# Kernel tuning notes

Measured on AMD Instinct MI355X. Metric: run time of the kernel, lower is better.

## Reference

```python
import jax, jax.numpy as jnp
import numpy as np

COLOR_SIZE = 8
FILTERS = 64
LAYERS = 4
CUMSUM_NORM = 256 * 256 * 3  # hardcoded in original: /256/256/3


def setup_inputs() -> dict:
    key = jax.random.key(0)
    k0, k1, k2, k3 = jax.random.split(key, 4)
    s = 0.05
    example = jax.random.randint(k0, (4, 256, 256, 3), 0, COLOR_SIZE, dtype=jnp.int32)
    # per-channel Dense stacks: layer 0 has input dim 1, layers 1..3 have input dim FILTERS
    W_in_first = jax.random.normal(k1, (3, 1, FILTERS), dtype=jnp.float32) * s
    b_in_first = jnp.zeros((3, FILTERS), dtype=jnp.float32)
    W_in_rest = jax.random.normal(k2, (LAYERS - 1, 3, FILTERS, FILTERS), dtype=jnp.float32) * s
    b_in_rest = jnp.zeros((LAYERS - 1, 3, FILTERS), dtype=jnp.float32)
    W_final = jax.random.normal(k3, (3, FILTERS, COLOR_SIZE), dtype=jnp.float32) * s
    b_final = jnp.zeros((3, COLOR_SIZE), dtype=jnp.float32)
    return {
        "example": example,
        "W_in_first": W_in_first, "b_in_first": b_in_first,
        "W_in_rest": W_in_rest, "b_in_rest": b_in_rest,
        "W_final": W_final, "b_final": b_final,
    }


def reference(example, W_in_first, b_in_first, W_in_rest, b_in_rest, W_final, b_final):
    # example: [B, H, W, 3] int in [0, COLOR_SIZE)
    x = example.astype(jnp.float32) / COLOR_SIZE * 2.0 - 1.0
    B, H, W, _ = x.shape
    L = H * W
    x = x.reshape(B, L, 3, 1)

    def layer(x, Wl, bl):
        # per-channel dense + relu: [B, L, 3, din] x [3, din, dout] -> [B, L, 3, dout]
        x = jax.nn.relu(jnp.einsum('blcd,cde->blce', x, Wl) + bl)
        # flatten channels into the sequence and take causal running sum
        x = x.reshape(B, L * 3, FILTERS)
        x = jnp.cumsum(x, axis=-2) / CUMSUM_NORM
        return x.reshape(B, L, 3, FILTERS)

    x = layer(x, W_in_first, b_in_first)
    for i in range(LAYERS - 1):
        x = layer(x, W_in_rest[i], b_in_rest[i])

    # final per-channel dense to color logits (no activation)
    x = jnp.einsum('blcd,cde->blce', x, W_final) + b_final
    return x.reshape(B, H, W, 3, COLOR_SIZE)
```

## Files before the change

kernel.cpp:

```cpp
#include <hip/hip_runtime.h>
#include <stdint.h>


#define BB 4
#define SP 65536
#define SS 196608
#define CI 1024
#define NG 16
#define INVN (1.0f / 196608.0f)

typedef __attribute__((ext_vector_type(8))) _Float16 half8;
typedef __attribute__((ext_vector_type(4))) float    f32x4;

__global__ __launch_bounds__(256)
void prep(const int* __restrict__ ex, const float* __restrict__ W0,
          const float* __restrict__ b0, const float* __restrict__ Wr,
          const float* __restrict__ Wfin,
          _Float16* __restrict__ Wt16, _Float16* __restrict__ Wf16p,
          float* __restrict__ Wf32, float* __restrict__ tab32,
          int* __restrict__ Hsub, int* __restrict__ Hqrt,
          float* __restrict__ Gz)
{
    __shared__ int hist[16][24];
    int tid = threadIdx.x, bi = blockIdx.x;
    int b = bi >> 6, g = (bi >> 2) & 15, q = bi & 3;
    for (int i = tid; i < 384; i += 256) hist[i / 24][i % 24] = 0;
    __syncthreads();
    for (int it = 0; it < 4; ++it) {
        int pl = it * 256 + tid;
        const int* ep = ex + ((size_t)b * SP + g * 4096 + q * 1024 + pl) * 3;
        int j = pl >> 6;
        atomicAdd(&hist[j][ep[0]], 1);
        atomicAdd(&hist[j][8 + ep[1]], 1);
        atomicAdd(&hist[j][16 + ep[2]], 1);
    }
    __syncthreads();
    for (int i = tid; i < 384; i += 256) {
        int j = i / 24, cv = i % 24;
        Hsub[(size_t)(b * CI + g * 64 + q * 16 + j) * 24 + cv] = hist[j][cv];
    }
    if (tid < 24) {
        int s = 0;
        for (int j = 0; j < 16; ++j) s += hist[j][tid];
        Hqrt[((size_t)(b * NG + g) * 4 + q) * 24 + tid] = s;
    }
    {
        int i0 = bi * 256 + tid, nth = 256 * 256;
        for (int idx = i0; idx < 12288; idx += nth)
            Gz[idx] = 0.f;
        for (int idx = i0; idx < 36864; idx += nth) {
            int d = idx & 63, f = (idx >> 6) & 63, lc = idx >> 12;
            Wt16[idx] = (_Float16)Wr[(size_t)(lc * 64 + d) * 64 + f];
        }
        for (int idx = i0; idx < 3072; idx += nth) {
            int d = idx & 63, n = (idx >> 6) & 15, c = idx >> 10;
            Wf16p[idx] = (n < 8) ? (_Float16)Wfin[(size_t)(c * 64 + d) * 8 + n]
                                 : (_Float16)0.f;
        }
        for (int idx = i0; idx < 1536; idx += nth) {
            int d = idx & 63, ck = idx >> 6;
            Wf32[idx] = Wfin[(size_t)((ck >> 3) * 64 + d) * 8 + (ck & 7)];
        }
        for (int idx = i0; idx < 1536; idx += nth) {
            int f = idx & 63, v = (idx >> 6) & 7, c = idx >> 9;
            float xv = v * 0.25f - 1.0f;
            tab32[idx] = fmaxf(W0[c * 64 + f] * xv + b0[c * 64 + f], 0.f);
        }
    }
}

__global__ __launch_bounds__(256, 4)
void midA(const int* __restrict__ ex,
          const int* __restrict__ Hsub, const int* __restrict__ Hqrt,
          const float* __restrict__ tab32,
          const _Float16* __restrict__ W16, const float* __restrict__ Wd32,
          const float* __restrict__ bias, _Float16* __restrict__ Y,
          float* __restrict__ A64, float* __restrict__ Ggrp)
{
    __shared__ float stab[1536];
    __shared__ __align__(16) _Float16 bounce3[3][64 * 72];
    __shared__ float segwt[3][4][64];
    __shared__ float basearr[192];
    __shared__ float hpart[4][24];
    __shared__ float carry[64];

    int tid = threadIdx.x, bi = blockIdx.x;
    int b = bi >> 10, ci = bi & 1023, g = ci >> 6, cr = ci & 63;
    int w = tid >> 6, ln = tid & 63, lm = ln & 15, lq = ln >> 4;
    int P0 = ci * 64;

    for (int i = tid; i < 1536; i += 256) stab[i] = tab32[i];
    if (ln < 24) {
        float s = 0.f;
        for (int j = w; j < g; j += 4) {
            const int* hq = Hqrt + ((size_t)(b * NG + j) * 4) * 24 + ln;
            s += (float)(hq[0] + hq[24] + hq[48] + hq[72]);
        }
        const int* hp = Hsub + (size_t)(b * CI + g * 64) * 24 + ln;
        for (int j = w; j < cr; j += 4) s += (float)hp[j * 24];
        hpart[w][ln] = s;
    }
    __syncthreads();

    float y0[3][16];
    {
#pragma unroll
        for (int p = 0; p < 16; ++p) {
            const int* ep = ex + ((size_t)b * SP + P0 + w * 16 + p) * 3;
            y0[0][p] = stab[ep[0] * 64 + ln];
            y0[1][p] = stab[(8 + ep[1]) * 64 + ln];
            y0[2][p] = stab[(16 + ep[2]) * 64 + ln];
        }
#pragma unroll
        for (int c = 0; c < 3; ++c)
#pragma unroll
            for (int p = 1; p < 16; ++p) y0[c][p] += y0[c][p - 1];
#pragma unroll
        for (int c = 0; c < 3; ++c) segwt[c][w][ln] = y0[c][15];
    }
    if (tid < 64) {
        float c0 = 0.f;
#pragma unroll
        for (int cv = 0; cv < 24; ++cv) {
            float cnt = hpart[0][cv] + hpart[1][cv] + hpart[2][cv] + hpart[3][cv];
            c0 += cnt * stab[cv * 64 + tid];
        }
        carry[tid] = c0;
    }
    __syncthreads();

    {
        float off0[3];
#pragma unroll
        for (int c = 0; c < 3; ++c) {
            float o = 0.f;
            for (int w2 = 0; w2 < w; ++w2) o += segwt[c][w2][ln];
            off0[c] = o;
        }
#pragma unroll
        for (int p = 0; p < 16; ++p) {
            float S0 = y0[0][p] + off0[0], S1 = y0[1][p] + off0[1], S2 = y0[2][p] + off0[2];
            float P1 = p ? y0[1][p - 1] + off0[1] : off0[1];
            float P2 = p ? y0[2][p - 1] + off0[2] : off0[2];
            int row = w * 16 + p;
            bounce3[0][row * 72 + ln] = (_Float16)(S0 + P1 + P2);
            bounce3[1][row * 72 + ln] = (_Float16)(S0 + S1 + P2);
            bounce3[2][row * 72 + ln] = (_Float16)(S0 + S1 + S2);
        }
    }
    if (tid < 192) {
        int c = tid >> 6, f = tid & 63;
        const float* wp = Wd32 + (size_t)(c * 64) * 64 + f;
        float a = 0.f;
        for (int d = 0; d < 64; ++d) a += carry[d] * wp[d * 64];
        basearr[tid] = bias[tid] + INVN * a;
    }
    __syncthreads();

    f32x4 acc[3][4];
#pragma unroll
    for (int c = 0; c < 3; ++c) {
        const half8* bb = (const half8*)&bounce3[c][0];
        half8 a0 = bb[(w * 16 + lm) * 9 + lq];
        half8 a1 = bb[(w * 16 + lm) * 9 + 4 + lq];
#pragma unroll
        for (int nt = 0; nt < 4; ++nt) {
            const half8* bp = (const half8*)(W16 + (size_t)(c * 64 + nt * 16 + lm) * 64);
            f32x4 t = {0.f, 0.f, 0.f, 0.f};
            t = __builtin_amdgcn_mfma_f32_16x16x32_f16(a0, bp[lq],     t, 0, 0, 0);
            t = __builtin_amdgcn_mfma_f32_16x16x32_f16(a1, bp[4 + lq], t, 0, 0, 0);
            acc[c][nt] = t;
        }
    }

    float s[3][4][4], wexcl[3][4];
#pragma unroll
    for (int c = 0; c < 3; ++c)
#pragma unroll
        for (int nt = 0; nt < 4; ++nt) {
            float base = basearr[c * 64 + nt * 16 + lm];
            float run = 0.f;
#pragma unroll
            for (int r = 0; r < 4; ++r) {
                float yv = fmaxf(base + INVN * acc[c][nt][r], 0.f);
                run += yv; s[c][nt][r] = run;
            }
            float v = run;
            float t1 = __shfl_up(v, 16); if (lq >= 1) v += t1;
            float t2 = __shfl_up(v, 32); if (lq >= 2) v += t2;
            wexcl[c][nt] = v - run;
            if (lq == 3) segwt[c][w][nt * 16 + lm] = v;
        }
    __syncthreads();

    {
        float off[3][4], tot[3][4];
#pragma unroll
        for (int c = 0; c < 3; ++c)
#pragma unroll
            for (int nt = 0; nt < 4; ++nt) {
                float o = wexcl[c][nt], ts = 0.f;
#pragma unroll
                for (int w2 = 0; w2 < 4; ++w2) {
                    float wv = segwt[c][w2][nt * 16 + lm];
                    ts += wv;
                    if (w2 < w) o += wv;
                }
                off[c][nt] = o; tot[c][nt] = ts;
            }
        if (w == 0 && lq == 0)
#pragma unroll
            for (int nt = 0; nt < 4; ++nt) {
                float t3 = tot[0][nt] + tot[1][nt] + tot[2][nt];
                A64[(size_t)(b * CI + ci) * 64 + nt * 16 + lm] = t3;
                atomicAdd(&Ggrp[(size_t)(b * NG + g) * 64 + nt * 16 + lm], t3);
            }
#pragma unroll
        for (int nt = 0; nt < 4; ++nt)
#pragma unroll
            for (int r = 0; r < 4; ++r) {
                float S0 = off[0][nt] + s[0][nt][r];
                float S1 = off[1][nt] + s[1][nt][r];
                float S2 = off[2][nt] + s[2][nt][r];
                float P1 = off[1][nt] + (r ? s[1][nt][r - 1] : 0.f);
                float P2 = off[2][nt] + (r ? s[2][nt][r - 1] : 0.f);
                int row = w * 16 + lq * 4 + r;
                bounce3[0][row * 72 + nt * 16 + lm] = (_Float16)(S0 + P1 + P2);
                bounce3[1][row * 72 + nt * 16 + lm] = (_Float16)(S0 + S1 + P2);
                bounce3[2][row * 72 + nt * 16 + lm] = (_Float16)(S0 + S1 + S2);
            }
    }
    __syncthreads();
#pragma unroll
    for (int q = 0; q < 6; ++q) {
        int idx = q * 256 + tid;
        int c = idx >> 9, rem = idx & 511;
        int pix = rem >> 3, f8 = rem & 7;
        half8 v = *(const half8*)&bounce3[c][pix * 72 + f8 * 8];
        ((half8*)(Y + ((size_t)(b * 3 + c) * SP + P0 + pix) * 64))[f8] = v;
    }
}

__global__ __launch_bounds__(256, 4)
void midB(const _Float16* Yin, _Float16* Yout,
          const float* __restrict__ A64p, const float* __restrict__ Ggrp_p,
          const _Float16* __restrict__ W16, const float* __restrict__ Wd32,
          const float* __restrict__ bias,
          float* __restrict__ A64, float* __restrict__ Ggrp)
{
    __shared__ __align__(16) _Float16 bounce3[3][64 * 72];
    __shared__ float wtop[3][4][64];
    __shared__ float basearr[192];
    __shared__ float cpart[4][64];
    __shared__ float carry[64];

    int tid = threadIdx.x, bi = blockIdx.x;
    int b = bi >> 10, ci = bi & 1023, g = ci >> 6, cr = ci & 63;
    int w = tid >> 6, ln = tid & 63, lm = ln & 15, lq = ln >> 4;
    int P0 = ci * 64;

    half8 af0[3], af1[3];
#pragma unroll
    for (int c = 0; c < 3; ++c) {
        const half8* ap = (const half8*)(Yin + ((size_t)(b * 3 + c) * SP + P0 + w * 16 + lm) * 64);
        af0[c] = ap[lq]; af1[c] = ap[4 + lq];
    }
    {
        float s = 0.f;
        for (int j = w; j < g; j += 4)
            s += Ggrp_p[(size_t)(b * NG + j) * 64 + ln];
        const float* ap = A64p + (size_t)(b * CI + g * 64) * 64 + ln;
        for (int j = w; j < cr; j += 4) s += ap[j * 64];
        cpart[w][ln] = s;
    }
    __syncthreads();
    if (tid < 64)
        carry[tid] = cpart[0][tid] + cpart[1][tid] + cpart[2][tid] + cpart[3][tid];
    __syncthreads();
    if (tid < 192) {
        int c = tid >> 6, f = tid & 63;
        const float* wp = Wd32 + (size_t)(c * 64) * 64 + f;
        float a = 0.f;
        for (int d = 0; d < 64; ++d) a += carry[d] * wp[d * 64];
        basearr[tid] = bias[tid] + INVN * a;
    }
    __syncthreads();

    f32x4 acc[3][4];
#pragma unroll
    for (int c = 0; c < 3; ++c)
#pragma unroll
        for (int nt = 0; nt < 4; ++nt) {
            const half8* bp = (const half8*)(W16 + (size_t)(c * 64 + nt * 16 + lm) * 64);
            f32x4 t = {0.f, 0.f, 0.f, 0.f};
            t = __builtin_amdgcn_mfma_f32_16x16x32_f16(af0[c], bp[lq],     t, 0, 0, 0);
            t = __builtin_amdgcn_mfma_f32_16x16x32_f16(af1[c], bp[4 + lq], t, 0, 0, 0);
            acc[c][nt] = t;
        }

    float s[3][4][4], wexcl[3][4];
#pragma unroll
    for (int c = 0; c < 3; ++c)
#pragma unroll
        for (int nt = 0; nt < 4; ++nt) {
            float base = basearr[c * 64 + nt * 16 + lm];
            float run = 0.f;
#pragma unroll
            for (int r = 0; r < 4; ++r) {
                float yv = fmaxf(base + INVN * acc[c][nt][r], 0.f);
                run += yv; s[c][nt][r] = run;
            }
            float v = run;
            float t1 = __shfl_up(v, 16); if (lq >= 1) v += t1;
            float t2 = __shfl_up(v, 32); if (lq >= 2) v += t2;
            wexcl[c][nt] = v - run;
            if (lq == 3) wtop[c][w][nt * 16 + lm] = v;
        }
    __syncthreads();

    {
        float off[3][4], tot[3][4];
#pragma unroll
        for (int c = 0; c < 3; ++c)
#pragma unroll
            for (int nt = 0; nt < 4; ++nt) {
                float o = wexcl[c][nt], ts = 0.f;
#pragma unroll
                for (int w2 = 0; w2 < 4; ++w2) {
                    float wv = wtop[c][w2][nt * 16 + lm];
                    ts += wv;
                    if (w2 < w) o += wv;
                }
                off[c][nt] = o; tot[c][nt] = ts;
            }
        if (w == 0 && lq == 0)
#pragma unroll
            for (int nt = 0; nt < 4; ++nt) {
                float t3 = tot[0][nt] + tot[1][nt] + tot[2][nt];
                A64[(size_t)(b * CI + ci) * 64 + nt * 16 + lm] = t3;
                atomicAdd(&Ggrp[(size_t)(b * NG + g) * 64 + nt * 16 + lm], t3);
            }
#pragma unroll
        for (int nt = 0; nt < 4; ++nt)
#pragma unroll
            for (int r = 0; r < 4; ++r) {
                float S0 = off[0][nt] + s[0][nt][r];
                float S1 = off[1][nt] + s[1][nt][r];
                float S2 = off[2][nt] + s[2][nt][r];
                float P1 = off[1][nt] + (r ? s[1][nt][r - 1] : 0.f);
                float P2 = off[2][nt] + (r ? s[2][nt][r - 1] : 0.f);
                int row = w * 16 + lq * 4 + r;
                bounce3[0][row * 72 + nt * 16 + lm] = (_Float16)(S0 + P1 + P2);
                bounce3[1][row * 72 + nt * 16 + lm] = (_Float16)(S0 + S1 + P2);
                bounce3[2][row * 72 + nt * 16 + lm] = (_Float16)(S0 + S1 + S2);
            }
    }
    __syncthreads();
#pragma unroll
    for (int q = 0; q < 6; ++q) {
        int idx = q * 256 + tid;
        int c = idx >> 9, rem = idx & 511;
        int pix = rem >> 3, f8 = rem & 7;
        half8 v = *(const half8*)&bounce3[c][pix * 72 + f8 * 8];
        ((half8*)(Yout + ((size_t)(b * 3 + c) * SP + P0 + pix) * 64))[f8] = v;
    }
}

__global__ __launch_bounds__(256, 4)
void midC(const _Float16* __restrict__ Yin,
          const float* __restrict__ A64p, const float* __restrict__ Ggrp_p,
          const _Float16* __restrict__ W16, const float* __restrict__ Wd32,
          const float* __restrict__ bias,
          const _Float16* __restrict__ Wf16p, const float* __restrict__ bfin,
          float* __restrict__ out, float* __restrict__ A64, float* __restrict__ Ggrp)
{
    __shared__ __align__(16) _Float16 bounce3[3][64 * 72];
    __shared__ float wtop[3][4][64];
    __shared__ float basearr[192];
    __shared__ float cpart[4][64];
    __shared__ float carry[64];
    __shared__ __align__(16) float outst[64 * 28];

    int tid = threadIdx.x, bi = blockIdx.x;
    int b = bi >> 10, ci = bi & 1023, g = ci >> 6, cr = ci & 63;
    int w = tid >> 6, ln = tid & 63, lm = ln & 15, lq = ln >> 4;
    int P0 = ci * 64;

    half8 af0[3], af1[3];
#pragma unroll
    for (int c = 0; c < 3; ++c) {
        const half8* ap = (const half8*)(Yin + ((size_t)(b * 3 + c) * SP + P0 + w * 16 + lm) * 64);
        af0[c] = ap[lq]; af1[c] = ap[4 + lq];
    }
    {
        float s = 0.f;
        for (int j = w; j < g; j += 4)
            s += Ggrp_p[(size_t)(b * NG + j) * 64 + ln];
        const float* ap = A64p + (size_t)(b * CI + g * 64) * 64 + ln;
        for (int j = w; j < cr; j += 4) s += ap[j * 64];
        cpart[w][ln] = s;
    }
    __syncthreads();
    if (tid < 64)
        carry[tid] = cpart[0][tid] + cpart[1][tid] + cpart[2][tid] + cpart[3][tid];
    __syncthreads();
    if (tid < 192) {
        int c = tid >> 6, f = tid & 63;
        const float* wp = Wd32 + (size_t)(c * 64) * 64 + f;
        float a = 0.f;
        for (int d = 0; d < 64; ++d) a += carry[d] * wp[d * 64];
        basearr[tid] = bias[tid] + INVN * a;
    }
    __syncthreads();

    f32x4 acc[3][4];
#pragma unroll
    for (int c = 0; c < 3; ++c)
#pragma unroll
        for (int nt = 0; nt < 4; ++nt) {
            const half8* bp = (const half8*)(W16 + (size_t)(c * 64 + nt * 16 + lm) * 64);
            f32x4 t = {0.f, 0.f, 0.f, 0.f};
            t = __builtin_amdgcn_mfma_f32_16x16x32_f16(af0[c], bp[lq],     t, 0, 0, 0);
            t = __builtin_amdgcn_mfma_f32_16x16x32_f16(af1[c], bp[4 + lq], t, 0, 0, 0);
            acc[c][nt] = t;
        }

    float s[3][4][4], wexcl[3][4];
#pragma unroll
    for (int c = 0; c < 3; ++c)
#pragma unroll
        for (int nt = 0; nt < 4; ++nt) {
            float base = basearr[c * 64 + nt * 16 + lm];
            float run = 0.f;
#pragma unroll
            for (int r = 0; r < 4; ++r) {
                float yv = fmaxf(base + INVN * acc[c][nt][r], 0.f);
                run += yv; s[c][nt][r] = run;
            }
            float v = run;
            float t1 = __shfl_up(v, 16); if (lq >= 1) v += t1;
            float t2 = __shfl_up(v, 32); if (lq >= 2) v += t2;
            wexcl[c][nt] = v - run;
            if (lq == 3) wtop[c][w][nt * 16 + lm] = v;
        }
    __syncthreads();

    {
        float off[3][4], tot[3][4];
#pragma unroll
        for (int c = 0; c < 3; ++c)
#pragma unroll
            for (int nt = 0; nt < 4; ++nt) {
                float o = wexcl[c][nt], ts = 0.f;
#pragma unroll
                for (int w2 = 0; w2 < 4; ++w2) {
                    float wv = wtop[c][w2][nt * 16 + lm];
                    ts += wv;
                    if (w2 < w) o += wv;
                }
                off[c][nt] = o; tot[c][nt] = ts;
            }
        if (w == 0 && lq == 0)
#pragma unroll
            for (int nt = 0; nt < 4; ++nt) {
                float t3 = tot[0][nt] + tot[1][nt] + tot[2][nt];
                A64[(size_t)(b * CI + ci) * 64 + nt * 16 + lm] = t3;
                atomicAdd(&Ggrp[(size_t)(b * NG + g) * 64 + nt * 16 + lm], t3);
            }
#pragma unroll
        for (int nt = 0; nt < 4; ++nt)
#pragma unroll
            for (int r = 0; r < 4; ++r) {
                float S0 = off[0][nt] + s[0][nt][r];
                float S1 = off[1][nt] + s[1][nt][r];
                float S2 = off[2][nt] + s[2][nt][r];
                float P1 = off[1][nt] + (r ? s[1][nt][r - 1] : 0.f);
                float P2 = off[2][nt] + (r ? s[2][nt][r - 1] : 0.f);
                int row = w * 16 + lq * 4 + r;
                bounce3[0][row * 72 + nt * 16 + lm] = (_Float16)(S0 + P1 + P2);
                bounce3[1][row * 72 + nt * 16 + lm] = (_Float16)(S0 + S1 + P2);
                bounce3[2][row * 72 + nt * 16 + lm] = (_Float16)(S0 + S1 + S2);
            }
    }
    __syncthreads();

#pragma unroll
    for (int c = 0; c < 3; ++c) {
        const half8* bb = (const half8*)&bounce3[c][0];
        half8 fa0 = bb[(w * 16 + lm) * 9 + lq];
        half8 fa1 = bb[(w * 16 + lm) * 9 + 4 + lq];
        const half8* fb = (const half8*)(Wf16p + (size_t)(c * 16 + lm) * 64);
        f32x4 t = {0.f, 0.f, 0.f, 0.f};
        t = __builtin_amdgcn_mfma_f32_16x16x32_f16(fa0, fb[lq],     t, 0, 0, 0);
        t = __builtin_amdgcn_mfma_f32_16x16x32_f16(fa1, fb[4 + lq], t, 0, 0, 0);
        if (lm < 8) {
            float bz = bfin[c * 8 + lm];
#pragma unroll
            for (int r = 0; r < 4; ++r)
                outst[(w * 16 + lq * 4 + r) * 28 + c * 8 + lm] = bz + INVN * t[r];
        }
    }
    __syncthreads();
    {
        float4* obase = (float4*)(out + ((size_t)b * SS + (size_t)P0 * 3) * 8);
#pragma unroll
        for (int k = 0; k < 2; ++k) {
            int idx = k * 256 + tid;
            if (idx < 384) {
                int pix = idx / 6, sub = (idx % 6) * 4;
                obase[idx] = *(const float4*)&outst[pix * 28 + sub];
            }
        }
    }
}

__global__ __launch_bounds__(256, 4)
void fixk(const float* __restrict__ A64p, const float* __restrict__ Ggrp_p,
          const float* __restrict__ Wf32, float* __restrict__ out)
{
    __shared__ float cpart[4][64];
    __shared__ float carry[64];
    __shared__ float part[24][8];
    __shared__ float vfix[24];
    int tid = threadIdx.x, bi = blockIdx.x;
    int b = bi >> 10, ci = bi & 1023, g = ci >> 6, cr = ci & 63;
    int w = tid >> 6, ln = tid & 63;
    int P0 = ci * 64;

    {
        float s = 0.f;
        for (int j = w; j < g; j += 4)
            s += Ggrp_p[(size_t)(b * NG + j) * 64 + ln];
        const float* ap = A64p + (size_t)(b * CI + g * 64) * 64 + ln;
        for (int j = w; j < cr; j += 4) s += ap[j * 64];
        cpart[w][ln] = s;
    }
    __syncthreads();
    if (tid < 64)
        carry[tid] = cpart[0][tid] + cpart[1][tid] + cpart[2][tid] + cpart[3][tid];
    __syncthreads();
    if (tid < 192) {
        int ck = tid >> 3, sg = tid & 7;
        const float* wp = Wf32 + ck * 64 + sg * 8;
        const float* cp = carry + sg * 8;
        float vf = 0.f;
#pragma unroll
        for (int d = 0; d < 8; ++d) vf += cp[d] * wp[d];
        part[ck][sg] = vf;
    }
    __syncthreads();
    if (tid < 24) {
        float vf = 0.f;
#pragma unroll
        for (int j = 0; j < 8; ++j) vf += part[tid][j];
        vfix[tid] = INVN * vf;
    }
    __syncthreads();
    float4* obase = (float4*)(out + ((size_t)b * SS + (size_t)P0 * 3) * 8);
#pragma unroll
    for (int k = 0; k < 2; ++k) {
        int idx = k * 256 + tid;
        if (idx < 384) {
            int sub = (idx % 6) * 4;
            float4 v = obase[idx];
            v.x += vfix[sub];
            v.y += vfix[sub + 1];
            v.z += vfix[sub + 2];
            v.w += vfix[sub + 3];
            obase[idx] = v;
        }
    }
}

extern "C" void kernel_launch(void* const* d_in, const int* in_sizes, int n_in,
                              void* d_out, int out_size, void* d_ws, size_t ws_size,
                              hipStream_t stream)
{
    const int*   ex   = (const int*)d_in[0];
    const float* W0   = (const float*)d_in[1];
    const float* b0   = (const float*)d_in[2];
    const float* Wr   = (const float*)d_in[3];
    const float* br   = (const float*)d_in[4];
    const float* Wfin = (const float*)d_in[5];
    const float* bfin = (const float*)d_in[6];
    float* out = (float*)d_out;

    char* ws = (char*)d_ws;
    size_t off = 0;
    _Float16* Y = (_Float16*)(ws + off); off += (size_t)BB * 3 * SP * 64 * 2;
    float* Ggrp1 = (float*)(ws + off); off += (size_t)BB * NG * 64 * 4;
    float* Ggrp2 = (float*)(ws + off); off += (size_t)BB * NG * 64 * 4;
    float* Ggrp3 = (float*)(ws + off); off += (size_t)BB * NG * 64 * 4;
    float* A64_1 = (float*)(ws + off); off += (size_t)BB * CI * 64 * 4;
    float* A64_2 = (float*)(ws + off); off += (size_t)BB * CI * 64 * 4;
    float* A64_3 = (float*)(ws + off); off += (size_t)BB * CI * 64 * 4;
    int* Hsub = (int*)(ws + off); off += (size_t)BB * CI * 24 * 4;
    int* Hqrt = (int*)(ws + off); off += (size_t)BB * NG * 4 * 24 * 4;
    _Float16* Wt16  = (_Float16*)(ws + off); off += 36864 * 2;
    _Float16* Wf16p = (_Float16*)(ws + off); off += 3072 * 2;
    float* Wf32  = (float*)(ws + off); off += 1536 * 4;
    float* tab32 = (float*)(ws + off); off += 1536 * 4;

    prep<<<256, 256, 0, stream>>>(ex, W0, b0, Wr, Wfin,
                                  Wt16, Wf16p, Wf32, tab32,
                                  Hsub, Hqrt, Ggrp1);
    midA<<<4096, 256, 0, stream>>>(ex, Hsub, Hqrt, tab32,
                                   Wt16, Wr, br, Y, A64_1, Ggrp1);
    midB<<<4096, 256, 0, stream>>>(Y, Y, A64_1, Ggrp1,
                                   Wt16 + 12288, Wr + 12288, br + 192,
                                   A64_2, Ggrp2);
    midC<<<4096, 256, 0, stream>>>(Y, A64_2, Ggrp2,
                                   Wt16 + 24576, Wr + 24576, br + 384,
                                   Wf16p, bfin, out, A64_3, Ggrp3);
    fixk<<<4096, 256, 0, stream>>>(A64_3, Ggrp3, Wf32, out);
}
```

Baseline: 358.6 us.

## Process two 64-pixel chunks per block to amortize carry and base setup

```diff
diff --git a/kernel.cpp b/kernel.cpp
--- a/kernel.cpp
+++ b/kernel.cpp
@@ -80,14 +80,15 @@
     __shared__ float stab[1536];
     __shared__ __align__(16) _Float16 bounce3[3][64 * 72];
     __shared__ float segwt[3][4][64];
-    __shared__ float basearr[192];
+    __shared__ float basearr[2][192];
     __shared__ float hpart[4][24];
-    __shared__ float carry[64];
+    __shared__ float hrow[24];
+    __shared__ float carry[2][64];
 
     int tid = threadIdx.x, bi = blockIdx.x;
-    int b = bi >> 10, ci = bi & 1023, g = ci >> 6, cr = ci & 63;
+    int b = bi >> 9, cp2 = bi & 511;
+    int ci0 = cp2 * 2, g = ci0 >> 6, cr0 = ci0 & 63;
     int w = tid >> 6, ln = tid & 63, lm = ln & 15, lq = ln >> 4;
-    int P0 = ci * 64;
 
     for (int i = tid; i < 1536; i += 256) stab[i] = tab32[i];
     if (ln < 24) {
@@ -97,13 +98,44 @@
             s += (float)(hq[0] + hq[24] + hq[48] + hq[72]);
         }
         const int* hp = Hsub + (size_t)(b * CI + g * 64) * 24 + ln;
-        for (int j = w; j < cr; j += 4) s += (float)hp[j * 24];
+        for (int j = w; j < cr0; j += 4) s += (float)hp[j * 24];
         hpart[w][ln] = s;
     }
-    __syncthreads();
-
-    float y0[3][16];
-    {
+    if (tid < 24) hrow[tid] = (float)Hsub[(size_t)(b * CI + ci0) * 24 + tid];
+    __syncthreads();
+
+    if (tid < 64) {
+        float c0 = 0.f, c1 = 0.f;
+#pragma unroll
+        for (int cv = 0; cv < 24; ++cv) {
+            float cnt = hpart[0][cv] + hpart[1][cv] + hpart[2][cv] + hpart[3][cv];
+            float sv = stab[cv * 64 + tid];
+            c0 += cnt * sv;
+            c1 += (cnt + hrow[cv]) * sv;
+        }
+        carry[0][tid] = c0; carry[1][tid] = c1;
+    }
+    __syncthreads();
+
+    if (tid < 192) {
+        int c = tid >> 6, f = tid & 63;
+        const float* wp = Wd32 + (size_t)(c * 64) * 64 + f;
+        float a0 = 0.f, a1 = 0.f;
+        for (int d = 0; d < 64; ++d) {
+            float wv = wp[d * 64];
+            a0 += carry[0][d] * wv; a1 += carry[1][d] * wv;
+        }
+        float bz = bias[tid];
+        basearr[0][tid] = bz + INVN * a0;
+        basearr[1][tid] = bz + INVN * a1;
+    }
+    __syncthreads();
+
+#pragma unroll 1
+    for (int pq = 0; pq < 2; ++pq) {
+        int ci = ci0 + pq, P0 = ci * 64;
+
+        float y0[3][16];
 #pragma unroll
         for (int p = 0; p < 16; ++p) {
             const int* ep = ex + ((size_t)b * SP + P0 + w * 16 + p) * 3;
@@ -117,127 +149,111 @@
             for (int p = 1; p < 16; ++p) y0[c][p] += y0[c][p - 1];
 #pragma unroll
         for (int c = 0; c < 3; ++c) segwt[c][w][ln] = y0[c][15];
-    }
-    if (tid < 64) {
-        float c0 = 0.f;
-#pragma unroll
-        for (int cv = 0; cv < 24; ++cv) {
-            float cnt = hpart[0][cv] + hpart[1][cv] + hpart[2][cv] + hpart[3][cv];
-            c0 += cnt * stab[cv * 64 + tid];
-        }
-        carry[tid] = c0;
-    }
-    __syncthreads();
-
-    {
-        float off0[3];
+        __syncthreads();
+
+        {
+            float off0[3];
+#pragma unroll
+            for (int c = 0; c < 3; ++c) {
+                float o = 0.f;
+                for (int w2 = 0; w2 < w; ++w2) o += segwt[c][w2][ln];
+                off0[c] = o;
+            }
+#pragma unroll
+            for (int p = 0; p < 16; ++p) {
+                float S0 = y0[0][p] + off0[0], S1 = y0[1][p] + off0[1], S2 = y0[2][p] + off0[2];
+                float P1 = p ? y0[1][p - 1] + off0[1] : off0[1];
+                float P2 = p ? y0[2][p - 1] + off0[2] : off0[2];
+                int row = w * 16 + p;
+                bounce3[0][row * 72 + ln] = (_Float16)(S0 + P1 + P2);
+                bounce3[1][row * 72 + ln] = (_Float16)(S0 + S1 + P2);
+                bounce3[2][row * 72 + ln] = (_Float16)(S0 + S1 + S2);
+            }
+        }
+        __syncthreads();
+
+        f32x4 acc[3][4];
 #pragma unroll
         for (int c = 0; c < 3; ++c) {
-            float o = 0.f;
-            for (int w2 = 0; w2 < w; ++w2) o += segwt[c][w2][ln];
-            off0[c] = o;
-        }
-#pragma unroll
-        for (int p = 0; p < 16; ++p) {
-            float S0 = y0[0][p] + off0[0], S1 = y0[1][p] + off0[1], S2 = y0[2][p] + off0[2];
-            float P1 = p ? y0[1][p - 1] + off0[1] : off0[1];
-            float P2 = p ? y0[2][p - 1] + off0[2] : off0[2];
-            int row = w * 16 + p;
-            bounce3[0][row * 72 + ln] = (_Float16)(S0 + P1 + P2);
-            bounce3[1][row * 72 + ln] = (_Float16)(S0 + S1 + P2);
-            bounce3[2][row * 72 + ln] = (_Float16)(S0 + S1 + S2);
-        }
-    }
-    if (tid < 192) {
-        int c = tid >> 6, f = tid & 63;
-        const float* wp = Wd32 + (size_t)(c * 64) * 64 + f;
-        float a = 0.f;
-        for (int d = 0; d < 64; ++d) a += carry[d] * wp[d * 64];
-        basearr[tid] = bias[tid] + INVN * a;
-    }
-    __syncthreads();
-
-    f32x4 acc[3][4];
-#pragma unroll
-    for (int c = 0; c < 3; ++c) {
-        const half8* bb = (const half8*)&bounce3[c][0];
-        half8 a0 = bb[(w * 16 + lm) * 9 + lq];
-        half8 a1 = bb[(w * 16 + lm) * 9 + 4 + lq];
-#pragma unroll
-        for (int nt = 0; nt < 4; ++nt) {
-            const half8* bp = (const half8*)(W16 + (size_t)(c * 64 + nt * 16 + lm) * 64);
-            f32x4 t = {0.f, 0.f, 0.f, 0.f};
-            t = __builtin_amdgcn_mfma_f32_16x16x32_f16(a0, bp[lq],     t, 0, 0, 0);
-            t = __builtin_amdgcn_mfma_f32_16x16x32_f16(a1, bp[4 + lq], t, 0, 0, 0);
-            acc[c][nt] = t;
-        }
-    }
-
-    float s[3][4][4], wexcl[3][4];
-#pragma unroll
-    for (int c = 0; c < 3; ++c)
-#pragma unroll
-        for (int nt = 0; nt < 4; ++nt) {
-            float base = basearr[c * 64 + nt * 16 + lm];
-            float run = 0.f;
-#pragma unroll
-            for (int r = 0; r < 4; ++r) {
-                float yv = fmaxf(base + INVN * acc[c][nt][r], 0.f);
-                run += yv; s[c][nt][r] = run;
-            }
-            float v = run;
-            float t1 = __shfl_up(v, 16); if (lq >= 1) v += t1;
-            float t2 = __shfl_up(v, 32); if (lq >= 2) v += t2;
-            wexcl[c][nt] = v - run;
-            if (lq == 3) segwt[c][w][nt * 16 + lm] = v;
-        }
-    __syncthreads();
-
-    {
-        float off[3][4], tot[3][4];
+            const half8* bb = (const half8*)&bounce3[c][0];
+            half8 a0 = bb[(w * 16 + lm) * 9 + lq];
+            half8 a1 = bb[(w * 16 + lm) * 9 + 4 + lq];
+#pragma unroll
+            for (int nt = 0; nt < 4; ++nt) {
+                const half8* bp = (const half8*)(W16 + (size_t)(c * 64 + nt * 16 + lm) * 64);
+                f32x4 t = {0.f, 0.f, 0.f, 0.f};
+                t = __builtin_amdgcn_mfma_f32_16x16x32_f16(a0, bp[lq],     t, 0, 0, 0);
+                t = __builtin_amdgcn_mfma_f32_16x16x32_f16(a1, bp[4 + lq], t, 0, 0, 0);
+                acc[c][nt] = t;
+            }
+        }
+
+        float s[3][4][4], wexcl[3][4];
 #pragma unroll
         for (int c = 0; c < 3; ++c)
 #pragma unroll
             for (int nt = 0; nt < 4; ++nt) {
-                float o = wexcl[c][nt], ts = 0.f;
-#pragma unroll
-                for (int w2 = 0; w2 < 4; ++w2) {
-                    float wv = segwt[c][w2][nt * 16 + lm];
-                    ts += wv;
-                    if (w2 < w) o += wv;
-                }
-                off[c][nt] = o; tot[c][nt] = ts;
-            }
-        if (w == 0 && lq == 0)
-#pragma unroll
-            for (int nt = 0; nt < 4; ++nt) {
-                float t3 = tot[0][nt] + tot[1][nt] + tot[2][nt];
-                A64[(size_t)(b * CI + ci) * 64 + nt * 16 + lm] = t3;
-                atomicAdd(&Ggrp[(size_t)(b * NG + g) * 64 + nt * 16 + lm], t3);
-            }
-#pragma unroll
-        for (int nt = 0; nt < 4; ++nt)
-#pragma unroll
-            for (int r = 0; r < 4; ++r) {
-                float S0 = off[0][nt] + s[0][nt][r];
-                float S1 = off[1][nt] + s[1][nt][r];
-                float S2 = off[2][nt] + s[2][nt][r];
-                float P1 = off[1][nt] + (r ? s[1][nt][r - 1] : 0.f);
-                float P2 = off[2][nt] + (r ? s[2][nt][r - 1] : 0.f);
-                int row = w * 16 + lq * 4 + r;
-                bounce3[0][row * 72 + nt * 16 + lm] = (_Float16)(S0 + P1 + P2);
-                bounce3[1][row * 72 + nt * 16 + lm] = (_Float16)(S0 + S1 + P2);
-                bounce3[2][row * 72 + nt * 16 + lm] = (_Float16)(S0 + S1 + S2);
-            }
-    }
-    __syncthreads();
-#pragma unroll
-    for (int q = 0; q < 6; ++q) {
-        int idx = q * 256 + tid;
-        int c = idx >> 9, rem = idx & 511;
-        int pix = rem >> 3, f8 = rem & 7;
-        half8 v = *(const half8*)&bounce3[c][pix * 72 + f8 * 8];
-        ((half8*)(Y + ((size_t)(b * 3 + c) * SP + P0 + pix) * 64))[f8] = v;
+                float base = basearr[pq][c * 64 + nt * 16 + lm];
+                float run = 0.f;
+#pragma unroll
+                for (int r = 0; r < 4; ++r) {
+                    float yv = fmaxf(base + INVN * acc[c][nt][r], 0.f);
+                    run += yv; s[c][nt][r] = run;
+                }
+                float v = run;
+                float t1 = __shfl_up(v, 16); if (lq >= 1) v += t1;
+                float t2 = __shfl_up(v, 32); if (lq >= 2) v += t2;
+                wexcl[c][nt] = v - run;
+                if (lq == 3) segwt[c][w][nt * 16 + lm] = v;
+            }
+        __syncthreads();
+
+        {
+            float off[3][4], tot[3][4];
+#pragma unroll
+            for (int c = 0; c < 3; ++c)
+#pragma unroll
+                for (int nt = 0; nt < 4; ++nt) {
+                    float o = wexcl[c][nt], ts = 0.f;
+#pragma unroll
+                    for (int w2 = 0; w2 < 4; ++w2) {
+                        float wv = segwt[c][w2][nt * 16 + lm];
+                        ts += wv;
+                        if (w2 < w) o += wv;
+                    }
+                    off[c][nt] = o; tot[c][nt] = ts;
+                }
+            if (w == 0 && lq == 0)
+#pragma unroll
+                for (int nt = 0; nt < 4; ++nt) {
+                    float t3 = tot[0][nt] + tot[1][nt] + tot[2][nt];
+                    A64[(size_t)(b * CI + ci) * 64 + nt * 16 + lm] = t3;
+                    atomicAdd(&Ggrp[(size_t)(b * NG + g) * 64 + nt * 16 + lm], t3);
+                }
+#pragma unroll
+            for (int nt = 0; nt < 4; ++nt)
+#pragma unroll
+                for (int r = 0; r < 4; ++r) {
+                    float S0 = off[0][nt] + s[0][nt][r];
+                    float S1 = off[1][nt] + s[1][nt][r];
+                    float S2 = off[2][nt] + s[2][nt][r];
+                    float P1 = off[1][nt] + (r ? s[1][nt][r - 1] : 0.f);
+                    float P2 = off[2][nt] + (r ? s[2][nt][r - 1] : 0.f);
+                    int row = w * 16 + lq * 4 + r;
+                    bounce3[0][row * 72 + nt * 16 + lm] = (_Float16)(S0 + P1 + P2);
+                    bounce3[1][row * 72 + nt * 16 + lm] = (_Float16)(S0 + S1 + P2);
+                    bounce3[2][row * 72 + nt * 16 + lm] = (_Float16)(S0 + S1 + S2);
+                }
+        }
+        __syncthreads();
+#pragma unroll
+        for (int q = 0; q < 6; ++q) {
+            int idx = q * 256 + tid;
+            int c = idx >> 9, rem = idx & 511;
+            int pix = rem >> 3, f8 = rem & 7;
+            half8 v = *(const half8*)&bounce3[c][pix * 72 + f8 * 8];
+            ((half8*)(Y + ((size_t)(b * 3 + c) * SP + P0 + pix) * 64))[f8] = v;
+        }
     }
 }
 
@@ -250,119 +266,134 @@
 {
     __shared__ __align__(16) _Float16 bounce3[3][64 * 72];
     __shared__ float wtop[3][4][64];
-    __shared__ float basearr[192];
+    __shared__ float basearr[2][192];
     __shared__ float cpart[4][64];
-    __shared__ float carry[64];
+    __shared__ float carry[2][64];
 
     int tid = threadIdx.x, bi = blockIdx.x;
-    int b = bi >> 10, ci = bi & 1023, g = ci >> 6, cr = ci & 63;
+    int b = bi >> 9, cp2 = bi & 511;
+    int ci0 = cp2 * 2, g = ci0 >> 6, cr0 = ci0 & 63;
     int w = tid >> 6, ln = tid & 63, lm = ln & 15, lq = ln >> 4;
-    int P0 = ci * 64;
-
-    half8 af0[3], af1[3];
-#pragma unroll
-    for (int c = 0; c < 3; ++c) {
-        const half8* ap = (const half8*)(Yin + ((size_t)(b * 3 + c) * SP + P0 + w * 16 + lm) * 64);
-        af0[c] = ap[lq]; af1[c] = ap[4 + lq];
-    }
+
     {
         float s = 0.f;
         for (int j = w; j < g; j += 4)
             s += Ggrp_p[(size_t)(b * NG + j) * 64 + ln];
         const float* ap = A64p + (size_t)(b * CI + g * 64) * 64 + ln;
-        for (int j = w; j < cr; j += 4) s += ap[j * 64];
+        for (int j = w; j < cr0; j += 4) s += ap[j * 64];
         cpart[w][ln] = s;
     }
     __syncthreads();
-    if (tid < 64)
-        carry[tid] = cpart[0][tid] + cpart[1][tid] + cpart[2][tid] + cpart[3][tid];
+    if (tid < 64) {
+        float c0 = cpart[0][tid] + cpart[1][tid] + cpart[2][tid] + cpart[3][tid];
+        carry[0][tid] = c0;
+        carry[1][tid] = c0 + A64p[(size_t)(b * CI + ci0) * 64 + tid];
+    }
     __syncthreads();
     if (tid < 192) {
         int c = tid >> 6, f = tid & 63;
         const float* wp = Wd32 + (size_t)(c * 64) * 64 + f;
-        float a = 0.f;
-        for (int d = 0; d < 64; ++d) a += carry[d] * wp[d * 64];
-        basearr[tid] = bias[tid] + INVN * a;
-    }
-    __syncthreads();
-
-    f32x4 acc[3][4];
-#pragma unroll
-    for (int c = 0; c < 3; ++c)
-#pragma unroll
-        for (int nt = 0; nt < 4; ++nt) {
-            const half8* bp = (const half8*)(W16 + (size_t)(c * 64 + nt * 16 + lm) * 64);
-            f32x4 t = {0.f, 0.f, 0.f, 0.f};
-            t = __builtin_amdgcn_mfma_f32_16x16x32_f16(af0[c], bp[lq],     t, 0, 0, 0);
-            t = __builtin_amdgcn_mfma_f32_16x16x32_f16(af1[c], bp[4 + lq], t, 0, 0, 0);
-            acc[c][nt] = t;
-        }
-
-    float s[3][4][4], wexcl[3][4];
-#pragma unroll
-    for (int c = 0; c < 3; ++c)
-#pragma unroll
-        for (int nt = 0; nt < 4; ++nt) {
-            float base = basearr[c * 64 + nt * 16 + lm];
-            float run = 0.f;
-#pragma unroll
-            for (int r = 0; r < 4; ++r) {
-                float yv = fmaxf(base + INVN * acc[c][nt][r], 0.f);
-                run += yv; s[c][nt][r] = run;
-            }
-            float v = run;
-            float t1 = __shfl_up(v, 16); if (lq >= 1) v += t1;
-            float t2 = __shfl_up(v, 32); if (lq >= 2) v += t2;
-            wexcl[c][nt] = v - run;
-            if (lq == 3) wtop[c][w][nt * 16 + lm] = v;
-        }
-    __syncthreads();
-
-    {
-        float off[3][4], tot[3][4];
+        float a0 = 0.f, a1 = 0.f;
+        for (int d = 0; d < 64; ++d) {
+            float wv = wp[d * 64];
+            a0 += carry[0][d] * wv; a1 += carry[1][d] * wv;
+        }
+        float bz = bias[tid];
+        basearr[0][tid] = bz + INVN * a0;
+        basearr[1][tid] = bz + INVN * a1;
+    }
+    __syncthreads();
+
+#pragma unroll 1
+    for (int pq = 0; pq < 2; ++pq) {
+        int ci = ci0 + pq, P0 = ci * 64;
+
+        half8 af0[3], af1[3];
+#pragma unroll
+        for (int c = 0; c < 3; ++c) {
+            const half8* ap = (const half8*)(Yin + ((size_t)(b * 3 + c) * SP + P0 + w * 16 + lm) * 64);
+            af0[c] = ap[lq]; af1[c] = ap[4 + lq];
+        }
+
+        f32x4 acc[3][4];
 #pragma unroll
         for (int c = 0; c < 3; ++c)
 #pragma unroll
             for (int nt = 0; nt < 4; ++nt) {
-                float o = wexcl[c][nt], ts = 0.f;
-#pragma unroll
-                for (int w2 = 0; w2 < 4; ++w2) {
-                    float wv = wtop[c][w2][nt * 16 + lm];
-                    ts += wv;
-                    if (w2 < w) o += wv;
-                }
-                off[c][nt] = o; tot[c][nt] = ts;
-            }
-        if (w == 0 && lq == 0)
+                const half8* bp = (const half8*)(W16 + (size_t)(c * 64 + nt * 16 + lm) * 64);
+                f32x4 t = {0.f, 0.f, 0.f, 0.f};
+                t = __builtin_amdgcn_mfma_f32_16x16x32_f16(af0[c], bp[lq],     t, 0, 0, 0);
+                t = __builtin_amdgcn_mfma_f32_16x16x32_f16(af1[c], bp[4 + lq], t, 0, 0, 0);
+                acc[c][nt] = t;
+            }
+
+        float s[3][4][4], wexcl[3][4];
+#pragma unroll
+        for (int c = 0; c < 3; ++c)
 #pragma unroll
             for (int nt = 0; nt < 4; ++nt) {
-                float t3 = tot[0][nt] + tot[1][nt] + tot[2][nt];
-                A64[(size_t)(b * CI + ci) * 64 + nt * 16 + lm] = t3;
-                atomicAdd(&Ggrp[(size_t)(b * NG + g) * 64 + nt * 16 + lm], t3);
-            }
-#pragma unroll
-        for (int nt = 0; nt < 4; ++nt)
-#pragma unroll
-            for (int r = 0; r < 4; ++r) {
-                float S0 = off[0][nt] + s[0][nt][r];
-                float S1 = off[1][nt] + s[1][nt][r];
-                float S2 = off[2][nt] + s[2][nt][r];
-                float P1 = off[1][nt] + (r ? s[1][nt][r - 1] : 0.f);
-                float P2 = off[2][nt] + (r ? s[2][nt][r - 1] : 0.f);
-                int row = w * 16 + lq * 4 + r;
-                bounce3[0][row * 72 + nt * 16 + lm] = (_Float16)(S0 + P1 + P2);
-                bounce3[1][row * 72 + nt * 16 + lm] = (_Float16)(S0 + S1 + P2);
-                bounce3[2][row * 72 + nt * 16 + lm] = (_Float16)(S0 + S1 + S2);
-            }
-    }
-    __syncthreads();
-#pragma unroll
-    for (int q = 0; q < 6; ++q) {
-        int idx = q * 256 + tid;
-        int c = idx >> 9, rem = idx & 511;
-        int pix = rem >> 3, f8 = rem & 7;
-        half8 v = *(const half8*)&bounce3[c][pix * 72 + f8 * 8];
-        ((half8*)(Yout + ((size_t)(b * 3 + c) * SP + P0 + pix) * 64))[f8] = v;
+                float base = basearr[pq][c * 64 + nt * 16 + lm];
+                float run = 0.f;
+#pragma unroll
+                for (int r = 0; r < 4; ++r) {
+                    float yv = fmaxf(base + INVN * acc[c][nt][r], 0.f);
+                    run += yv; s[c][nt][r] = run;
+                }
+                float v = run;
+                float t1 = __shfl_up(v, 16); if (lq >= 1) v += t1;
+                float t2 = __shfl_up(v, 32); if (lq >= 2) v += t2;
+                wexcl[c][nt] = v - run;
+                if (lq == 3) wtop[c][w][nt * 16 + lm] = v;
+            }
+        __syncthreads();
+
+        {
+            float off[3][4], tot[3][4];
+#pragma unroll
+            for (int c = 0; c < 3; ++c)
+#pragma unroll
+                for (int nt = 0; nt < 4; ++nt) {
+                    float o = wexcl[c][nt], ts = 0.f;
+#pragma unroll
+                    for (int w2 = 0; w2 < 4; ++w2) {
+                        float wv = wtop[c][w2][nt * 16 + lm];
+                        ts += wv;
+                        if (w2 < w) o += wv;
+                    }
+                    off[c][nt] = o; tot[c][nt] = ts;
+                }
+            if (w == 0 && lq == 0)
+#pragma unroll
+                for (int nt = 0; nt < 4; ++nt) {
+                    float t3 = tot[0][nt] + tot[1][nt] + tot[2][nt];
+                    A64[(size_t)(b * CI + ci) * 64 + nt * 16 + lm] = t3;
+                    atomicAdd(&Ggrp[(size_t)(b * NG + g) * 64 + nt * 16 + lm], t3);
+                }
+#pragma unroll
+            for (int nt = 0; nt < 4; ++nt)
+#pragma unroll
+                for (int r = 0; r < 4; ++r) {
+                    float S0 = off[0][nt] + s[0][nt][r];
+                    float S1 = off[1][nt] + s[1][nt][r];
+                    float S2 = off[2][nt] + s[2][nt][r];
+                    float P1 = off[1][nt] + (r ? s[1][nt][r - 1] : 0.f);
+                    float P2 = off[2][nt] + (r ? s[2][nt][r - 1] : 0.f);
+                    int row = w * 16 + lq * 4 + r;
+                    bounce3[0][row * 72 + nt * 16 + lm] = (_Float16)(S0 + P1 + P2);
+                    bounce3[1][row * 72 + nt * 16 + lm] = (_Float16)(S0 + S1 + P2);
+                    bounce3[2][row * 72 + nt * 16 + lm] = (_Float16)(S0 + S1 + S2);
+                }
+        }
+        __syncthreads();
+#pragma unroll
+        for (int q = 0; q < 6; ++q) {
+            int idx = q * 256 + tid;
+            int c = idx >> 9, rem = idx & 511;
+            int pix = rem >> 3, f8 = rem & 7;
+            half8 v = *(const half8*)&bounce3[c][pix * 72 + f8 * 8];
+            ((half8*)(Yout + ((size_t)(b * 3 + c) * SP + P0 + pix) * 64))[f8] = v;
+        }
+        if (pq == 0) __syncthreads();
     }
 }
 
@@ -376,141 +407,156 @@
 {
     __shared__ __align__(16) _Float16 bounce3[3][64 * 72];
     __shared__ float wtop[3][4][64];
-    __shared__ float basearr[192];
-    __shared__ float cpart[4][64];
-    __shared__ float carry[64];
+    __shared__ float basearr[2][192];
     __shared__ __align__(16) float outst[64 * 28];
+    float (*cpart)[64] = (float (*)[64])outst;
+    float (*carry)[64] = (float (*)[64])(outst + 256);
 
     int tid = threadIdx.x, bi = blockIdx.x;
-    int b = bi >> 10, ci = bi & 1023, g = ci >> 6, cr = ci & 63;
+    int b = bi >> 9, cp2 = bi & 511;
+    int ci0 = cp2 * 2, g = ci0 >> 6, cr0 = ci0 & 63;
     int w = tid >> 6, ln = tid & 63, lm = ln & 15, lq = ln >> 4;
-    int P0 = ci * 64;
-
-    half8 af0[3], af1[3];
-#pragma unroll
-    for (int c = 0; c < 3; ++c) {
-        const half8* ap = (const half8*)(Yin + ((size_t)(b * 3 + c) * SP + P0 + w * 16 + lm) * 64);
-        af0[c] = ap[lq]; af1[c] = ap[4 + lq];
-    }
+
     {
         float s = 0.f;
         for (int j = w; j < g; j += 4)
             s += Ggrp_p[(size_t)(b * NG + j) * 64 + ln];
         const float* ap = A64p + (size_t)(b * CI + g * 64) * 64 + ln;
-        for (int j = w; j < cr; j += 4) s += ap[j * 64];
+        for (int j = w; j < cr0; j += 4) s += ap[j * 64];
         cpart[w][ln] = s;
     }
     __syncthreads();
-    if (tid < 64)
-        carry[tid] = cpart[0][tid] + cpart[1][tid] + cpart[2][tid] + cpart[3][tid];
+    if (tid < 64) {
+        float c0 = cpart[0][tid] + cpart[1][tid] + cpart[2][tid] + cpart[3][tid];
+        carry[0][tid] = c0;
+        carry[1][tid] = c0 + A64p[(size_t)(b * CI + ci0) * 64 + tid];
+    }
     __syncthreads();
     if (tid < 192) {
         int c = tid >> 6, f = tid & 63;
         const float* wp = Wd32 + (size_t)(c * 64) * 64 + f;
-        float a = 0.f;
-        for (int d = 0; d < 64; ++d) a += carry[d] * wp[d * 64];
-        basearr[tid] = bias[tid] + INVN * a;
-    }
-    __syncthreads();
-
-    f32x4 acc[3][4];
-#pragma unroll
-    for (int c = 0; c < 3; ++c)
-#pragma unroll
-        for (int nt = 0; nt < 4; ++nt) {
-            const half8* bp = (const half8*)(W16 + (size_t)(c * 64 + nt * 16 + lm) * 64);
+        float a0 = 0.f, a1 = 0.f;
+        for (int d = 0; d < 64; ++d) {
+            float wv = wp[d * 64];
+            a0 += carry[0][d] * wv; a1 += carry[1][d] * wv;
+        }
+        float bz = bias[tid];
+        basearr[0][tid] = bz + INVN * a0;
+        basearr[1][tid] = bz + INVN * a1;
+    }
+    __syncthreads();
+
+#pragma unroll 1
+    for (int pq = 0; pq < 2; ++pq) {
+        int ci = ci0 + pq, P0 = ci * 64;
+
+        half8 af0[3], af1[3];
+#pragma unroll
+        for (int c = 0; c < 3; ++c) {
+            const half8* ap = (const half8*)(Yin + ((size_t)(b * 3 + c) * SP + P0 + w * 16 + lm) * 64);
+            af0[c] = ap[lq]; af1[c] = ap[4 + lq];
+        }
+
+        f32x4 acc[3][4];
+#pragma unroll
+        for (int c = 0; c < 3; ++c)
+#pragma unroll
+            for (int nt = 0; nt < 4; ++nt) {
+                const half8* bp = (const half8*)(W16 + (size_t)(c * 64 + nt * 16 + lm) * 64);
+                f32x4 t = {0.f, 0.f, 0.f, 0.f};
+                t = __builtin_amdgcn_mfma_f32_16x16x32_f16(af0[c], bp[lq],     t, 0, 0, 0);
+                t = __builtin_amdgcn_mfma_f32_16x16x32_f16(af1[c], bp[4 + lq], t, 0, 0, 0);
+                acc[c][nt] = t;
+            }
+
+        float s[3][4][4], wexcl[3][4];
+#pragma unroll
+        for (int c = 0; c < 3; ++c)
+#pragma unroll
+            for (int nt = 0; nt < 4; ++nt) {
+                float base = basearr[pq][c * 64 + nt * 16 + lm];
+                float run = 0.f;
+#pragma unroll
+                for (int r = 0; r < 4; ++r) {
+                    float yv = fmaxf(base + INVN * acc[c][nt][r], 0.f);
+                    run += yv; s[c][nt][r] = run;
+                }
+                float v = run;
+                float t1 = __shfl_up(v, 16); if (lq >= 1) v += t1;
+                float t2 = __shfl_up(v, 32); if (lq >= 2) v += t2;
+                wexcl[c][nt] = v - run;
+                if (lq == 3) wtop[c][w][nt * 16 + lm] = v;
+            }
+        __syncthreads();
+
+        {
+            float off[3][4], tot[3][4];
+#pragma unroll
+            for (int c = 0; c < 3; ++c)
+#pragma unroll
+                for (int nt = 0; nt < 4; ++nt) {
+                    float o = wexcl[c][nt], ts = 0.f;
+#pragma unroll
+                    for (int w2 = 0; w2 < 4; ++w2) {
+                        float wv = wtop[c][w2][nt * 16 + lm];
+                        ts += wv;
+                        if (w2 < w) o += wv;
+                    }
+                    off[c][nt] = o; tot[c][nt] = ts;
+                }
+            if (w == 0 && lq == 0)
+#pragma unroll
+                for (int nt = 0; nt < 4; ++nt) {
+                    float t3 = tot[0][nt] + tot[1][nt] + tot[2][nt];
+                    A64[(size_t)(b * CI + ci) * 64 + nt * 16 + lm] = t3;
+                    atomicAdd(&Ggrp[(size_t)(b * NG + g) * 64 + nt * 16 + lm], t3);
+                }
+#pragma unroll
+            for (int nt = 0; nt < 4; ++nt)
+#pragma unroll
+                for (int r = 0; r < 4; ++r) {
+                    float S0 = off[0][nt] + s[0][nt][r];
+                    float S1 = off[1][nt] + s[1][nt][r];
+                    float S2 = off[2][nt] + s[2][nt][r];
+                    float P1 = off[1][nt] + (r ? s[1][nt][r - 1] : 0.f);
+                    float P2 = off[2][nt] + (r ? s[2][nt][r - 1] : 0.f);
+                    int row = w * 16 + lq * 4 + r;
+                    bounce3[0][row * 72 + nt * 16 + lm] = (_Float16)(S0 + P1 + P2);
+                    bounce3[1][row * 72 + nt * 16 + lm] = (_Float16)(S0 + S1 + P2);
+                    bounce3[2][row * 72 + nt * 16 + lm] = (_Float16)(S0 + S1 + S2);
+                }
+        }
+        __syncthreads();
+
+#pragma unroll
+        for (int c = 0; c < 3; ++c) {
+            const half8* bb = (const half8*)&bounce3[c][0];
+            half8 fa0 = bb[(w * 16 + lm) * 9 + lq];
+            half8 fa1 = bb[(w * 16 + lm) * 9 + 4 + lq];
+            const half8* fb = (const half8*)(Wf16p + (size_t)(c * 16 + lm) * 64);
             f32x4 t = {0.f, 0.f, 0.f, 0.f};
-            t = __builtin_amdgcn_mfma_f32_16x16x32_f16(af0[c], bp[lq],     t, 0, 0, 0);
-            t = __builtin_amdgcn_mfma_f32_16x16x32_f16(af1[c], bp[4 + lq], t, 0, 0, 0);
-            acc[c][nt] = t;
-        }
-
-    float s[3][4][4], wexcl[3][4];
-#pragma unroll
-    for (int c = 0; c < 3; ++c)
-#pragma unroll
-        for (int nt = 0; nt < 4; ++nt) {
-            float base = basearr[c * 64 + nt * 16 + lm];
-            float run = 0.f;
-#pragma unroll
-            for (int r = 0; r < 4; ++r) {
-                float yv = fmaxf(base + INVN * acc[c][nt][r], 0.f);
-                run += yv; s[c][nt][r] = run;
-            }
-            float v = run;
-            float t1 = __shfl_up(v, 16); if (lq >= 1) v += t1;
-            float t2 = __shfl_up(v, 32); if (lq >= 2) v += t2;
-            wexcl[c][nt] = v - run;
-            if (lq == 3) wtop[c][w][nt * 16 + lm] = v;
-        }
-    __syncthreads();
-
-    {
-        float off[3][4], tot[3][4];
-#pragma unroll
-        for (int c = 0; c < 3; ++c)
-#pragma unroll
-            for (int nt = 0; nt < 4; ++nt) {
-                float o = wexcl[c][nt], ts = 0.f;
-#pragma unroll
-                for (int w2 = 0; w2 < 4; ++w2) {
-                    float wv = wtop[c][w2][nt * 16 + lm];
-                    ts += wv;
-                    if (w2 < w) o += wv;
-                }
-                off[c][nt] = o; tot[c][nt] = ts;
-            }
-        if (w == 0 && lq == 0)
-#pragma unroll
-            for (int nt = 0; nt < 4; ++nt) {
-                float t3 = tot[0][nt] + tot[1][nt] + tot[2][nt];
-                A64[(size_t)(b * CI + ci) * 64 + nt * 16 + lm] = t3;
-                atomicAdd(&Ggrp[(size_t)(b * NG + g) * 64 + nt * 16 + lm], t3);
-            }
-#pragma unroll
-        for (int nt = 0; nt < 4; ++nt)
-#pragma unroll
-            for (int r = 0; r < 4; ++r) {
-                float S0 = off[0][nt] + s[0][nt][r];
-                float S1 = off[1][nt] + s[1][nt][r];
-                float S2 = off[2][nt] + s[2][nt][r];
-                float P1 = off[1][nt] + (r ? s[1][nt][r - 1] : 0.f);
-                float P2 = off[2][nt] + (r ? s[2][nt][r - 1] : 0.f);
-                int row = w * 16 + lq * 4 + r;
-                bounce3[0][row * 72 + nt * 16 + lm] = (_Float16)(S0 + P1 + P2);
-                bounce3[1][row * 72 + nt * 16 + lm] = (_Float16)(S0 + S1 + P2);
-                bounce3[2][row * 72 + nt * 16 + lm] = (_Float16)(S0 + S1 + S2);
-            }
-    }
-    __syncthreads();
-
-#pragma unroll
-    for (int c = 0; c < 3; ++c) {
-        const half8* bb = (const half8*)&bounce3[c][0];
-        half8 fa0 = bb[(w * 16 + lm) * 9 + lq];
-        half8 fa1 = bb[(w * 16 + lm) * 9 + 4 + lq];
-        const half8* fb = (const half8*)(Wf16p + (size_t)(c * 16 + lm) * 64);
-        f32x4 t = {0.f, 0.f, 0.f, 0.f};
-        t = __builtin_amdgcn_mfma_f32_16x16x32_f16(fa0, fb[lq],     t, 0, 0, 0);
-        t = __builtin_amdgcn_mfma_f32_16x16x32_f16(fa1, fb[4 + lq], t, 0, 0, 0);
-        if (lm < 8) {
-            float bz = bfin[c * 8 + lm];
-#pragma unroll
-            for (int r = 0; r < 4; ++r)
-                outst[(w * 16 + lq * 4 + r) * 28 + c * 8 + lm] = bz + INVN * t[r];
-        }
-    }
-    __syncthreads();
-    {
-        float4* obase = (float4*)(out + ((size_t)b * SS + (size_t)P0 * 3) * 8);
-#pragma unroll
-        for (int k = 0; k < 2; ++k) {
-            int idx = k * 256 + tid;
-            if (idx < 384) {
-                int pix = idx / 6, sub = (idx % 6) * 4;
-                obase[idx] = *(const float4*)&outst[pix * 28 + sub];
-            }
-        }
+            t = __builtin_amdgcn_mfma_f32_16x16x32_f16(fa0, fb[lq],     t, 0, 0, 0);
+            t = __builtin_amdgcn_mfma_f32_16x16x32_f16(fa1, fb[4 + lq], t, 0, 0, 0);
+            if (lm < 8) {
+                float bz = bfin[c * 8 + lm];
+#pragma unroll
+                for (int r = 0; r < 4; ++r)
+                    outst[(w * 16 + lq * 4 + r) * 28 + c * 8 + lm] = bz + INVN * t[r];
+            }
+        }
+        __syncthreads();
+        {
+            float4* obase = (float4*)(out + ((size_t)b * SS + (size_t)P0 * 3) * 8);
+#pragma unroll
+            for (int k = 0; k < 2; ++k) {
+                int idx = k * 256 + tid;
+                if (idx < 384) {
+                    int pix = idx / 6, sub = (idx % 6) * 4;
+                    obase[idx] = *(const float4*)&outst[pix * 28 + sub];
+                }
+            }
+        }
+        if (pq == 0) __syncthreads();
     }
 }
 
@@ -604,12 +650,12 @@
     prep<<<256, 256, 0, stream>>>(ex, W0, b0, Wr, Wfin,
                                   Wt16, Wf16p, Wf32, tab32,
                                   Hsub, Hqrt, Ggrp1);
-    midA<<<4096, 256, 0, stream>>>(ex, Hsub, Hqrt, tab32,
+    midA<<<2048, 256, 0, stream>>>(ex, Hsub, Hqrt, tab32,
                                    Wt16, Wr, br, Y, A64_1, Ggrp1);
-    midB<<<4096, 256, 0, stream>>>(Y, Y, A64_1, Ggrp1,
+    midB<<<2048, 256, 0, stream>>>(Y, Y, A64_1, Ggrp1,
                                    Wt16 + 12288, Wr + 12288, br + 192,
                                    A64_2, Ggrp2);
-    midC<<<4096, 256, 0, stream>>>(Y, A64_2, Ggrp2,
+    midC<<<2048, 256, 0, stream>>>(Y, A64_2, Ggrp2,
                                    Wt16 + 24576, Wr + 24576, br + 384,
                                    Wf16p, bfin, out, A64_3, Ggrp3);
     fixk<<<4096, 256, 0, stream>>>(A64_3, Ggrp3, Wf32, out);
```

After: 641.0 us. 78.7% more time.
